# Optimization experiments

Hardware: AMD Instinct MI355X
Metric: run time of the kernel (lower is better)

## Reference

```python
import jax, jax.numpy as jnp
import numpy as np

NUM_EMB = 1024
EMB_DIM = 256
BETA = 0.25


def setup_inputs() -> dict:
    key = jax.random.key(0)
    k1, k2 = jax.random.split(key)
    z = jax.random.normal(k1, (64, 32, 32, EMB_DIM), dtype=jnp.float32)
    # RandomUniform(-1/N, 1/N) init, shape (embedding_dimension, number_embeddings)
    embeddings = jax.random.uniform(
        k2, (EMB_DIM, NUM_EMB), dtype=jnp.float32,
        minval=-1.0 / NUM_EMB, maxval=1.0 / NUM_EMB)
    return {"z": z, "embeddings": embeddings}


def reference(z, embeddings):
    beta = BETA
    z_flat = z.reshape(-1, EMB_DIM)                      # [N, D]
    # squared L2 distances via ||z||^2 + ||e||^2 - 2 z @ e
    distances = (jnp.sum(z_flat ** 2, axis=1, keepdims=True)
                 + jnp.sum(embeddings ** 2, axis=0)
                 - 2.0 * (z_flat @ embeddings))          # [N, K]
    encoding_indices = jnp.argmin(distances, axis=1)     # [N] int
    quantized = embeddings.T[encoding_indices].reshape(z.shape)  # gather rows of e^T
    vq_loss = jnp.mean((quantized - jax.lax.stop_gradient(z)) ** 2)
    commitment_loss = beta * jnp.mean((jax.lax.stop_gradient(quantized) - z) ** 2)
    quantized_st = z + jax.lax.stop_gradient(quantized - z)  # straight-through
    # perplexity from codebook usage histogram
    counts = jnp.zeros((NUM_EMB,), dtype=distances.dtype).at[encoding_indices].add(1.0)
    avg_probs = counts / encoding_indices.shape[0]
    perplexity = jnp.exp(-jnp.sum(avg_probs * jnp.log(avg_probs + 1e-10)))
    return (quantized_st, encoding_indices, vq_loss, commitment_loss, perplexity)
```

## Files before the change

kernel.cpp:

```cpp
#include <hip/hip_runtime.h>
#include <math.h>

#define NUM_EMB 1024
#define EMB_DIM 256
#define NROWS   65536
#define NTHREADS 256
#define MTHREADS 1024
#define EPSF 1.5e-3f
#define GCAP 458752
#define LLCAP 3837

#define OFF_IDX  16777216
#define OFF_VQ   16842752

#define WS_C2    0
#define WS_HIST  4096
#define WS_LOSS  8192
#define WS_GCNT  8196
#define WS_R2    8448
#define WS_SLOT  270592
#define WS_ETF   794880
#define WS_ETB   1843456
#define WS_RMIN  2367744
#define WS_GLIST 2629888

typedef __attribute__((ext_vector_type(8))) short bf16x8;
typedef __attribute__((ext_vector_type(4))) float f32x4;

__device__ __forceinline__ unsigned short f2bf(float x) {
  unsigned u = __float_as_uint(x);
  unsigned r = (u + 0x7FFFu + ((u >> 16) & 1u)) >> 16;
  return (unsigned short)r;
}

__global__ __launch_bounds__(NTHREADS) void vq_pt(
    const float* __restrict__ emb, float* __restrict__ cvec,
    int* __restrict__ hist, float* __restrict__ loss, int* __restrict__ gcnt,
    float* __restrict__ embTf, unsigned short* __restrict__ embTbf) {
  __shared__ float t[64][65];
  const int tid = threadIdx.x;
  if (blockIdx.x < 4) {
    int k = blockIdx.x * NTHREADS + tid;
    float s = 0.f;
    for (int d = 0; d < EMB_DIM; ++d) {
      float v = emb[d * NUM_EMB + k];
      s = __fadd_rn(s, __fmul_rn(v, v));
    }
    cvec[k] = s;
    hist[k] = 0;
    if (k == 0) { *loss = 0.f; *gcnt = 0; }
  } else {
    const int b = blockIdx.x - 4;
    const int kt = b & 15, dt = b >> 4;
    #pragma unroll
    for (int it = 0; it < 16; ++it) {
      int i = tid + it * NTHREADS, r = i >> 6, c = i & 63;
      t[r][c] = emb[(dt * 64 + r) * NUM_EMB + kt * 64 + c];
    }
    __syncthreads();
    #pragma unroll
    for (int it = 0; it < 16; ++it) {
      int i = tid + it * NTHREADS, r = i >> 6, c = i & 63;
      float v = t[c][r];
      embTf[(kt * 64 + r) * EMB_DIM + dt * 64 + c] = v;
      embTbf[(kt * 64 + r) * EMB_DIM + dt * 64 + c] = f2bf(v);
    }
  }
}

__global__ __launch_bounds__(NTHREADS) void vq_r2k(
    const float* __restrict__ z, float* __restrict__ r2out) {
  __shared__ float zc[64][36];
  __shared__ float pmm[64][2][4];
  const int tid = threadIdx.x;
  const int n0 = blockIdx.x * 64;
  const float* zrow = z + (size_t)n0 * EMB_DIM;
  const int prow = tid >> 2, pm = tid & 3;
  float racc[2][2] = {{0.f, 0.f}, {0.f, 0.f}};
  for (int dc = 0; dc < 8; ++dc) {
    __syncthreads();
    #pragma unroll
    for (int it = 0; it < 2; ++it) {
      int i = tid + it * NTHREADS, row = i >> 3, f4 = i & 7;
      *(float4*)(&zc[row][f4 * 4]) = *(const float4*)(zrow + row * EMB_DIM + dc * 32 + f4 * 4);
    }
    __syncthreads();
    const int half = dc >> 2;
    #pragma unroll
    for (int q = 0; q < 4; ++q)
      #pragma unroll
      for (int jj = 0; jj < 2; ++jj) {
        float v = zc[prow][(pm * 2 + jj) + 8 * q];
        racc[half][jj] = __fadd_rn(racc[half][jj], __fmul_rn(v, v));
      }
  }
  pmm[prow][0][pm] = __fadd_rn(racc[0][0], racc[0][1]);
  pmm[prow][1][pm] = __fadd_rn(racc[1][0], racc[1][1]);
  __syncthreads();
  if (tid < 64) {
    float h0 = __fadd_rn(__fadd_rn(pmm[tid][0][0], pmm[tid][0][1]),
                         __fadd_rn(pmm[tid][0][2], pmm[tid][0][3]));
    float h1 = __fadd_rn(__fadd_rn(pmm[tid][1][0], pmm[tid][1][1]),
                         __fadd_rn(pmm[tid][1][2], pmm[tid][1][3]));
    r2out[n0 + tid] = __fadd_rn(h0, h1);
  }
}

__global__ __launch_bounds__(MTHREADS) void vq_mfma(
    const float* __restrict__ z, const unsigned short* __restrict__ embTbf,
    const float* __restrict__ cvec, unsigned long long* __restrict__ slots,
    int* __restrict__ gcnt, unsigned int* __restrict__ glist,
    int* __restrict__ grm) {
  __shared__ unsigned short zc[256][256];
  __shared__ unsigned short Bl[2][8192];

  int* caps = (int*)&Bl[1][0];
  unsigned int* llist = (unsigned int*)caps + 259;

  const int tid = threadIdx.x;
  const int lane = tid & 63, wave = tid >> 6;
  const int quad = lane >> 4, l15 = lane & 15;
  const int rg = wave >> 2, cg = wave & 3;
  const int n0 = blockIdx.x * 256;

  if (tid < 256) {
    grm[n0 + tid] = 0x7F000000;
    slots[n0 + tid] = ~0ULL;
  }

  #pragma unroll
  for (int it = 0; it < 8; ++it) {
    int g = tid + it * MTHREADS, row = g >> 5, u = g & 31;
    const float* src = z + (size_t)(n0 + row) * EMB_DIM + u * 8;
    float4 a = *(const float4*)src;
    float4 b = *(const float4*)(src + 4);
    uint4 w;
    w.x = ((unsigned)f2bf(a.y) << 16) | f2bf(a.x);
    w.y = ((unsigned)f2bf(a.w) << 16) | f2bf(a.z);
    w.z = ((unsigned)f2bf(b.y) << 16) | f2bf(b.x);
    w.w = ((unsigned)f2bf(b.w) << 16) | f2bf(b.z);
    *(uint4*)(&zc[row][(u ^ (row & 7)) * 8]) = w;
  }

  const int bn = tid >> 2, bseg = tid & 3;
  const size_t bofs = (size_t)bn * EMB_DIM + (size_t)bseg * 8;
  uint4 p0 = *(const uint4*)(embTbf + bofs);
  __syncthreads();
  *(uint4*)(&Bl[0][(size_t)tid * 8]) = p0;
  uint4 bpre = *(const uint4*)(embTbf + 32 + bofs);
  __syncthreads();

  for (int j = 0; j < 4; ++j) {
    f32x4 acc[4][4];
    #pragma unroll
    for (int rt = 0; rt < 4; ++rt)
      #pragma unroll
      for (int ct = 0; ct < 4; ++ct)
        acc[rt][ct] = (f32x4){0.f, 0.f, 0.f, 0.f};
    float c2r[4];
    #pragma unroll
    for (int ct = 0; ct < 4; ++ct)
      c2r[ct] = cvec[j * 256 + cg * 64 + ct * 16 + l15] + 1.0f;

    for (int kc = 0; kc < 8; ++kc) {
      const int c = j * 8 + kc;
      if (c < 31)
        *(uint4*)(&Bl[(c + 1) & 1][(size_t)tid * 8]) = bpre;
      if (c + 2 < 32)
        bpre = *(const uint4*)(embTbf + (size_t)((c + 2) >> 3) * 65536 +
                               (size_t)((c + 2) & 7) * 32 + bofs);
      bf16x8 av[4], bv[4];
      #pragma unroll
      for (int rt = 0; rt < 4; ++rt) {
        int row = rg * 64 + rt * 16 + l15;
        av[rt] = *(const bf16x8*)(&zc[row][((kc * 4 + quad) ^ (l15 & 7)) * 8]);
      }
      #pragma unroll
      for (int ct = 0; ct < 4; ++ct)
        bv[ct] = *(const bf16x8*)(&Bl[c & 1][(size_t)((cg * 64 + ct * 16 + l15) * 32 + quad * 8)]);
      #pragma unroll
      for (int rt = 0; rt < 4; ++rt)
        #pragma unroll
        for (int ct = 0; ct < 4; ++ct)
          acc[rt][ct] = __builtin_amdgcn_mfma_f32_16x16x32_bf16(av[rt], bv[ct], acc[rt][ct], 0, 0, 0);
      __syncthreads();
    }
    if (tid < 256) caps[tid] = 0x7F000000;
    if (tid == 0) caps[256] = 0;
    __syncthreads();

    #pragma unroll
    for (int rt = 0; rt < 4; ++rt)
      #pragma unroll
      for (int reg = 0; reg < 4; ++reg) {
        float m = 1e30f;
        #pragma unroll
        for (int ct = 0; ct < 4; ++ct) {
          float d = fmaf(-2.f, acc[rt][ct][reg], c2r[ct]);
          m = fminf(m, d);
        }
        #pragma unroll
        for (int off = 1; off < 16; off <<= 1)
          m = fminf(m, __shfl_xor(m, off));
        if (l15 == 0)
          atomicMin(&caps[rg * 64 + rt * 16 + quad * 4 + reg], __float_as_int(m));
      }
    __syncthreads();

    if (tid < 256) {
      int lm = caps[tid];
      int old = atomicMin(&grm[n0 + tid], lm);
      caps[tid] = lm < old ? lm : old;
    }
    __syncthreads();

    #pragma unroll
    for (int rt = 0; rt < 4; ++rt)
      #pragma unroll
      for (int reg = 0; reg < 4; ++reg) {
        int rowl = rg * 64 + rt * 16 + quad * 4 + reg;
        float fmin = __int_as_float(caps[rowl]);
        #pragma unroll
        for (int ct = 0; ct < 4; ++ct) {
          float d = fmaf(-2.f, acc[rt][ct][reg], c2r[ct]);
          if (d <= fmin + EPSF) {
            int k = j * 256 + cg * 64 + ct * 16 + l15;
            int id = atomicAdd(&caps[256], 1);
            if (id < LLCAP) llist[id] = ((unsigned)(n0 + rowl) << 10) | (unsigned)k;
          }
        }
      }
    __syncthreads();
    if (tid == 0) {
      int c = caps[256]; if (c > LLCAP) c = LLCAP;
      caps[258] = c;
      caps[257] = atomicAdd(gcnt, c);
    }
    __syncthreads();
    {
      int cnt = caps[258], base = caps[257];
      for (int i = tid; i < cnt; i += MTHREADS)
        if (base + i < GCAP) glist[base + i] = llist[i];
    }
    __syncthreads();
  }
}

__global__ __launch_bounds__(NTHREADS) void vq_refine(
    const float* __restrict__ z, const float* __restrict__ embTf,
    const float* __restrict__ r2, const float* __restrict__ cvec,
    const int* __restrict__ gcnt, const unsigned int* __restrict__ glist,
    unsigned long long* __restrict__ slots) {
  int n = *gcnt; if (n > GCAP) n = GCAP;
  for (int i = blockIdx.x * NTHREADS + threadIdx.x; i < n;
       i += gridDim.x * NTHREADS) {
    unsigned e = glist[i];
    int grow = (int)(e >> 10), k = (int)(e & 1023);
    const float* zr = z + (size_t)grow * EMB_DIM;
    const float* er = embTf + (size_t)k * EMB_DIM;
    float s = 0.f;
    for (int d = 0; d < EMB_DIM; ++d)
      s = fmaf(zr[d], er[d], s);
    float dist = __fsub_rn(__fadd_rn(r2[grow], cvec[k]), __fmul_rn(2.0f, s));
    unsigned long long key =
        ((unsigned long long)__float_as_uint(dist) << 32) | (unsigned)k;
    atomicMin(&slots[grow], key);
  }
}

__global__ __launch_bounds__(NTHREADS) void vq_epi(
    const float* __restrict__ z, const float* __restrict__ embTf,
    const unsigned long long* __restrict__ slots,
    float* __restrict__ out, int* __restrict__ hist, float* __restrict__ loss) {
  __shared__ int ks[64];
  __shared__ float wsum[4];
  const int tid = threadIdx.x;
  const int n0 = blockIdx.x * 64;
  const float* zrow = z + (size_t)n0 * EMB_DIM;
  if (tid < 64) {
    int k = (int)(slots[n0 + tid] & 1023ULL);
    ks[tid] = k;
    out[OFF_IDX + n0 + tid] = (float)k;
    atomicAdd(&hist[k], 1);
  }
  __syncthreads();
  float sumsq = 0.f;
  #pragma unroll
  for (int it = 0; it < 16; ++it) {
    int g = tid + it * NTHREADS;
    int row = g >> 6;
    int d = (g & 63) * 4;
    int k = ks[row];
    float4 zv = *(const float4*)(zrow + row * EMB_DIM + d);
    float4 q = *(const float4*)(embTf + (size_t)k * EMB_DIM + d);
    float4 df;
    df.x = q.x - zv.x; df.y = q.y - zv.y; df.z = q.z - zv.z; df.w = q.w - zv.w;
    sumsq = fmaf(df.x, df.x, sumsq);
    sumsq = fmaf(df.y, df.y, sumsq);
    sumsq = fmaf(df.z, df.z, sumsq);
    sumsq = fmaf(df.w, df.w, sumsq);
    *(float4*)(out + (size_t)(n0 + row) * EMB_DIM + d) = q;
  }
  #pragma unroll
  for (int off = 32; off > 0; off >>= 1) sumsq += __shfl_down(sumsq, off);
  if ((tid & 63) == 0) wsum[tid >> 6] = sumsq;
  __syncthreads();
  if (tid == 0) atomicAdd(loss, wsum[0] + wsum[1] + wsum[2] + wsum[3]);
}

__global__ __launch_bounds__(NTHREADS) void vq_finalize(
    const int* __restrict__ hist, const float* __restrict__ loss,
    float* __restrict__ out) {
  __shared__ float ws[4];
  int tid = threadIdx.x;
  float s = 0.f;
  for (int k = tid; k < NUM_EMB; k += NTHREADS) {
    float p = (float)hist[k] * (1.0f / 65536.0f);
    s += p * logf(p + 1e-10f);
  }
  #pragma unroll
  for (int off = 32; off > 0; off >>= 1) s += __shfl_down(s, off);
  if ((tid & 63) == 0) ws[tid >> 6] = s;
  __syncthreads();
  if (tid == 0) {
    float tot = ws[0] + ws[1] + ws[2] + ws[3];
    float vq = *loss * (1.0f / 16777216.0f);
    out[OFF_VQ + 0] = vq;
    out[OFF_VQ + 1] = 0.25f * vq;
    out[OFF_VQ + 2] = expf(-tot);
  }
}

extern "C" void kernel_launch(void* const* d_in, const int* in_sizes, int n_in,
                              void* d_out, int out_size, void* d_ws, size_t ws_size,
                              hipStream_t stream) {
  const float* z   = (const float*)d_in[0];
  const float* emb = (const float*)d_in[1];
  float* out = (float*)d_out;
  char* ws = (char*)d_ws;
  float* cvec   = (float*)(ws + WS_C2);
  int*   hist   = (int*)(ws + WS_HIST);
  float* loss   = (float*)(ws + WS_LOSS);
  int*   gcnt   = (int*)(ws + WS_GCNT);
  float* r2     = (float*)(ws + WS_R2);
  unsigned long long* slots = (unsigned long long*)(ws + WS_SLOT);
  float* embTf  = (float*)(ws + WS_ETF);
  unsigned short* embTbf = (unsigned short*)(ws + WS_ETB);
  int*   grm    = (int*)(ws + WS_RMIN);
  unsigned int* glist = (unsigned int*)(ws + WS_GLIST);

  vq_pt<<<68, NTHREADS, 0, stream>>>(emb, cvec, hist, loss, gcnt, embTf, embTbf);
  vq_r2k<<<NROWS / 64, NTHREADS, 0, stream>>>(z, r2);
  vq_mfma<<<NROWS / 256, MTHREADS, 0, stream>>>(z, embTbf, cvec, slots, gcnt, glist, grm);
  vq_refine<<<512, NTHREADS, 0, stream>>>(z, embTf, r2, cvec, gcnt, glist, slots);
  vq_epi<<<NROWS / 64, NTHREADS, 0, stream>>>(z, embTf, slots, out, hist, loss);
  vq_finalize<<<1, NTHREADS, 0, stream>>>(hist, loss, out);
}
```

Before: 284.0 us.

## Swizzle codebook LDS tile, use LDS-only barriers, aggregate candidate atomics

Adds an XOR swizzle to the layout of the bf16 codebook tile in shared memory to reduce bank conflicts on the MFMA operand reads. Every __syncthreads is replaced with a barrier that waits only on LDS/scalar counters, so the in-flight global prefetch of the next codebook chunk is not drained at each barrier. Candidate-list appends now use wavefront ballot plus one shared atomicAdd per wave instead of one atomic per lane. The risk is that barriers no longer order global memory operations.

```diff
diff --git a/kernel.cpp b/kernel.cpp
--- a/kernel.cpp
+++ b/kernel.cpp
@@ -26,6 +26,12 @@
 
 typedef __attribute__((ext_vector_type(8))) short bf16x8;
 typedef __attribute__((ext_vector_type(4))) float f32x4;
+
+#define BAR_LGKM() do {                                        \
+    asm volatile("s_waitcnt lgkmcnt(0)" ::: "memory");         \
+    __builtin_amdgcn_s_barrier();                              \
+    asm volatile("" ::: "memory");                             \
+  } while (0)
 
 __device__ __forceinline__ unsigned short f2bf(float x) {
   unsigned u = __float_as_uint(x);
@@ -144,11 +150,19 @@
 
   const int bn = tid >> 2, bseg = tid & 3;
   const size_t bofs = (size_t)bn * EMB_DIM + (size_t)bseg * 8;
+  const int bunit = bn * 4 + (bseg ^ ((bn >> 1) & 3));
+  int bidx[4];
+  #pragma unroll
+  for (int ct = 0; ct < 4; ++ct) {
+    int cn = cg * 64 + ct * 16 + l15;
+    bidx[ct] = (cn * 4 + (quad ^ ((cn >> 1) & 3))) * 8;
+  }
+
   uint4 p0 = *(const uint4*)(embTbf + bofs);
-  __syncthreads();
-  *(uint4*)(&Bl[0][(size_t)tid * 8]) = p0;
+  BAR_LGKM();
+  *(uint4*)(&Bl[0][(size_t)bunit * 8]) = p0;
   uint4 bpre = *(const uint4*)(embTbf + 32 + bofs);
-  __syncthreads();
+  BAR_LGKM();
 
   for (int j = 0; j < 4; ++j) {
     f32x4 acc[4][4];
@@ -165,7 +179,7 @@
     for (int kc = 0; kc < 8; ++kc) {
       const int c = j * 8 + kc;
       if (c < 31)
-        *(uint4*)(&Bl[(c + 1) & 1][(size_t)tid * 8]) = bpre;
+        *(uint4*)(&Bl[(c + 1) & 1][(size_t)bunit * 8]) = bpre;
       if (c + 2 < 32)
         bpre = *(const uint4*)(embTbf + (size_t)((c + 2) >> 3) * 65536 +
                                (size_t)((c + 2) & 7) * 32 + bofs);
@@ -177,17 +191,17 @@
       }
       #pragma unroll
       for (int ct = 0; ct < 4; ++ct)
-        bv[ct] = *(const bf16x8*)(&Bl[c & 1][(size_t)((cg * 64 + ct * 16 + l15) * 32 + quad * 8)]);
+        bv[ct] = *(const bf16x8*)(&Bl[c & 1][(size_t)bidx[ct]]);
       #pragma unroll
       for (int rt = 0; rt < 4; ++rt)
         #pragma unroll
         for (int ct = 0; ct < 4; ++ct)
           acc[rt][ct] = __builtin_amdgcn_mfma_f32_16x16x32_bf16(av[rt], bv[ct], acc[rt][ct], 0, 0, 0);
-      __syncthreads();
+      BAR_LGKM();
     }
     if (tid < 256) caps[tid] = 0x7F000000;
     if (tid == 0) caps[256] = 0;
-    __syncthreads();
+    BAR_LGKM();
 
     #pragma unroll
     for (int rt = 0; rt < 4; ++rt)
@@ -205,14 +219,14 @@
         if (l15 == 0)
           atomicMin(&caps[rg * 64 + rt * 16 + quad * 4 + reg], __float_as_int(m));
       }
-    __syncthreads();
+    BAR_LGKM();
 
     if (tid < 256) {
       int lm = caps[tid];
       int old = atomicMin(&grm[n0 + tid], lm);
       caps[tid] = lm < old ? lm : old;
     }
-    __syncthreads();
+    BAR_LGKM();
 
     #pragma unroll
     for (int rt = 0; rt < 4; ++rt)
@@ -223,26 +237,36 @@
         #pragma unroll
         for (int ct = 0; ct < 4; ++ct) {
           float d = fmaf(-2.f, acc[rt][ct][reg], c2r[ct]);
-          if (d <= fmin + EPSF) {
-            int k = j * 256 + cg * 64 + ct * 16 + l15;
-            int id = atomicAdd(&caps[256], 1);
-            if (id < LLCAP) llist[id] = ((unsigned)(n0 + rowl) << 10) | (unsigned)k;
+          bool pred = (d <= fmin + EPSF);
+          unsigned long long msk = __ballot(pred);
+          if (msk) {
+            int leader = (int)(__ffsll((long long)msk) - 1);
+            int cnt = (int)__popcll(msk);
+            int base0 = 0;
+            if (lane == leader) base0 = atomicAdd(&caps[256], cnt);
+            base0 = __shfl(base0, leader);
+            if (pred) {
+              int id = base0 + (int)__popcll(msk & ((1ULL << lane) - 1ULL));
+              int k = j * 256 + cg * 64 + ct * 16 + l15;
+              if (id < LLCAP)
+                llist[id] = ((unsigned)(n0 + rowl) << 10) | (unsigned)k;
+            }
           }
         }
       }
-    __syncthreads();
+    BAR_LGKM();
     if (tid == 0) {
       int c = caps[256]; if (c > LLCAP) c = LLCAP;
       caps[258] = c;
       caps[257] = atomicAdd(gcnt, c);
     }
-    __syncthreads();
+    BAR_LGKM();
     {
       int cnt = caps[258], base = caps[257];
       for (int i = tid; i < cnt; i += MTHREADS)
         if (base + i < GCAP) glist[base + i] = llist[i];
     }
-    __syncthreads();
+    BAR_LGKM();
   }
 }
 
```

Result: slower. 290.0 us (+2.1%).
